# Kernel optimization log

Measured on AMD Instinct MI355X. Metric: run time of the kernel, lower is better.

Reference implementation:

```python
import jax, jax.numpy as jnp
import numpy as np

NUM_EXPERTS = 8
TOP_K = 2


def setup_inputs() -> dict:
    key = jax.random.key(0)
    ks = jax.random.split(key, 8)
    B, S, D, H, E = 4, 2048, 1024, 2048, NUM_EXPERTS
    sd = 1.0 / np.sqrt(D)
    sh = 1.0 / np.sqrt(H)
    return {
        "x": jax.random.normal(ks[0], (B, S, D), dtype=jnp.float32),
        "noise": jax.random.normal(ks[1], (B, S, E), dtype=jnp.float32),
        "router_w": jax.random.normal(ks[2], (E, D), dtype=jnp.float32) * sd,
        "router_b": jnp.zeros((E,), dtype=jnp.float32),
        "noise_w": jax.random.normal(ks[3], (E, D), dtype=jnp.float32) * sd,
        "noise_b": jnp.zeros((E,), dtype=jnp.float32),
        "w1": jax.random.normal(ks[4], (E, H, D), dtype=jnp.float32) * sd,
        "w2": jax.random.normal(ks[5], (E, D, H), dtype=jnp.float32) * sh,
        "w3": jax.random.normal(ks[6], (E, H, D), dtype=jnp.float32) * sd,
    }


def reference(x, noise, router_w, router_b, noise_w, noise_b, w1, w2, w3):
    B, S, D = x.shape
    T = B * S
    xf = x.reshape(T, D)                                  # [T, D]
    noise_f = noise.reshape(T, -1)                        # [T, E]

    # Noisy top-k router
    logits = xf @ router_w.T + router_b                   # [T, E]
    noise_logits = xf @ noise_w.T + noise_b               # [T, E]
    noisy = logits + noise_f * jax.nn.softplus(noise_logits)
    top_vals, top_idx = jax.lax.top_k(noisy, TOP_K)       # [T, K]
    sparse = jnp.full_like(noisy, -jnp.inf)
    sparse = sparse.at[jnp.arange(T)[:, None], top_idx].set(top_vals)
    gates = jax.nn.softmax(sparse, axis=-1)               # [T, E]; zero off top-k

    # Expert SwiGLU combine. Gates are exactly 0 for non-selected experts, so
    # the masked gather/scatter loop of the original equals this weighted sum.
    out = jnp.zeros_like(xf)
    for i in range(NUM_EXPERTS):
        h = jax.nn.silu(xf @ w1[i].T) * (xf @ w3[i].T)    # [T, H]
        out = out + gates[:, i:i + 1] * (h @ w2[i].T)     # [T, D]
    return out.reshape(B, S, D)
```

## Files before the change

kernel.cpp:

```cpp
#include <hip/hip_runtime.h>

typedef unsigned short u16;
typedef __attribute__((ext_vector_type(8))) __bf16 bf16x8;
typedef __attribute__((ext_vector_type(8))) short short8;
typedef __attribute__((ext_vector_type(4))) float f32x4;

#define NE 8

__device__ __forceinline__ u16 f2bf(float f) {
    union { float f; unsigned u; } v; v.f = f;
    unsigned u = v.u;
    return (u16)((u + 0x7fffu + ((u >> 16) & 1u)) >> 16);
}

__device__ __forceinline__ f32x4 mfma16(short8 a, short8 b, f32x4 c) {
    return __builtin_amdgcn_mfma_f32_16x16x32_bf16(
        __builtin_bit_cast(bf16x8, a), __builtin_bit_cast(bf16x8, b), c, 0, 0, 0);
}

__device__ __forceinline__ void gl2lds(const u16* g, u16* l) {
    __builtin_amdgcn_global_load_lds((const __attribute__((address_space(1))) void*)g,
                                     (__attribute__((address_space(3))) void*)l,
                                     16, 0, 0);
}

__global__ void cvt_kernel(const float* __restrict__ in, u16* __restrict__ out, size_t n4) {
    size_t i = (size_t)blockIdx.x * blockDim.x + threadIdx.x;
    size_t stride = (size_t)gridDim.x * blockDim.x;
    for (; i < n4; i += stride) {
        float4 v = ((const float4*)in)[i];
        ushort4 o;
        o.x = f2bf(v.x); o.y = f2bf(v.y); o.z = f2bf(v.z); o.w = f2bf(v.w);
        ((ushort4*)out)[i] = o;
    }
}

__global__ void cvt_w13_kernel(const float* __restrict__ w1, const float* __restrict__ w3,
                               u16* __restrict__ wc, int H, int D) {
    size_t n = (size_t)NE * H * (D / 4);
    size_t i = (size_t)blockIdx.x * blockDim.x + threadIdx.x;
    size_t stride = (size_t)gridDim.x * blockDim.x;
    int d4n = D / 4;
    for (; i < n; i += stride) {
        int d4 = (int)(i % d4n);
        size_t rem = i / d4n;
        int j = (int)(rem % H);
        int e = (int)(rem / H);
        float4 v1 = ((const float4*)w1)[i];
        float4 v3 = ((const float4*)w3)[i];
        ushort4 o1, o3;
        o1.x = f2bf(v1.x); o1.y = f2bf(v1.y); o1.z = f2bf(v1.z); o1.w = f2bf(v1.w);
        o3.x = f2bf(v3.x); o3.y = f2bf(v3.y); o3.z = f2bf(v3.z); o3.w = f2bf(v3.w);
        int wcrow = ((j >> 4) << 5) + (j & 15);
        size_t o = (((size_t)e * 2 * H + wcrow) * d4n + d4);
        ((ushort4*)wc)[o] = o1;
        ((ushort4*)wc)[o + (size_t)16 * d4n] = o3;
    }
}

__global__ void router_kernel(const float* __restrict__ x, const float* __restrict__ noise,
                              const float* __restrict__ rw, const float* __restrict__ rb,
                              const float* __restrict__ nw, const float* __restrict__ nb,
                              int* __restrict__ tops, float* __restrict__ gpair,
                              u16* __restrict__ xb, int T, int D) {
    int wv = threadIdx.x >> 6;
    int lane = threadIdx.x & 63;
    int t = blockIdx.x * 4 + wv;
    if (t >= T) return;

    const float4* x4 = (const float4*)(x + (size_t)t * D) + lane * 4;
    float4 xv0 = x4[0], xv1 = x4[1], xv2 = x4[2], xv3 = x4[3];

    {
        ushort4 s0, s1, s2, s3;
        s0.x = f2bf(xv0.x); s0.y = f2bf(xv0.y); s0.z = f2bf(xv0.z); s0.w = f2bf(xv0.w);
        s1.x = f2bf(xv1.x); s1.y = f2bf(xv1.y); s1.z = f2bf(xv1.z); s1.w = f2bf(xv1.w);
        s2.x = f2bf(xv2.x); s2.y = f2bf(xv2.y); s2.z = f2bf(xv2.z); s2.w = f2bf(xv2.w);
        s3.x = f2bf(xv3.x); s3.y = f2bf(xv3.y); s3.z = f2bf(xv3.z); s3.w = f2bf(xv3.w);
        ushort4* o = (ushort4*)(xb + (size_t)t * D + lane * 16);
        o[0] = s0; o[1] = s1; o[2] = s2; o[3] = s3;
    }

    float acc[2 * NE];
#pragma unroll
    for (int e = 0; e < NE; e++) {
        const float4* w4 = (const float4*)(rw + (size_t)e * D) + lane * 4;
        float4 a = w4[0], b = w4[1], c = w4[2], d = w4[3];
        acc[e] = xv0.x*a.x + xv0.y*a.y + xv0.z*a.z + xv0.w*a.w
               + xv1.x*b.x + xv1.y*b.y + xv1.z*b.z + xv1.w*b.w
               + xv2.x*c.x + xv2.y*c.y + xv2.z*c.z + xv2.w*c.w
               + xv3.x*d.x + xv3.y*d.y + xv3.z*d.z + xv3.w*d.w;
        const float4* v4 = (const float4*)(nw + (size_t)e * D) + lane * 4;
        a = v4[0]; b = v4[1]; c = v4[2]; d = v4[3];
        acc[NE + e] = xv0.x*a.x + xv0.y*a.y + xv0.z*a.z + xv0.w*a.w
                    + xv1.x*b.x + xv1.y*b.y + xv1.z*b.z + xv1.w*b.w
                    + xv2.x*c.x + xv2.y*c.y + xv2.z*c.z + xv2.w*c.w
                    + xv3.x*d.x + xv3.y*d.y + xv3.z*d.z + xv3.w*d.w;
    }
#pragma unroll
    for (int m = 1; m < 64; m <<= 1) {
#pragma unroll
        for (int k = 0; k < 2 * NE; k++) acc[k] += __shfl_xor(acc[k], m);
    }

    if (lane == 0) {
        float v0 = -1e30f, v1 = -1e30f;
        int i0 = 0, i1 = 0;
#pragma unroll
        for (int e = 0; e < NE; e++) {
            float z = acc[NE + e] + nb[e];
            float sp = (z > 20.f) ? z : log1pf(expf(z));
            float nv = acc[e] + rb[e] + noise[(size_t)t * NE + e] * sp;
            if (nv > v0) { v1 = v0; i1 = i0; v0 = nv; i0 = e; }
            else if (nv > v1) { v1 = nv; i1 = e; }
        }
        float e1 = expf(v1 - v0);
        float inv = 1.f / (1.f + e1);
        tops[t] = i0 | (i1 << 8);
        gpair[2 * t]     = inv;
        gpair[2 * t + 1] = e1 * inv;
    }
}

__global__ void build_kernel(const int* __restrict__ tops, const float* __restrict__ gpair,
                             int* __restrict__ counts, int* __restrict__ list,
                             float* __restrict__ glist, int* __restrict__ tokslot, int T) {
    int e = blockIdx.x;
    int tid = threadIdx.x, lane = tid & 63, wv = tid >> 6;
    __shared__ int wsum[4];
    __shared__ int sbase;
    if (tid == 0) sbase = 0;
    __syncthreads();
    for (int t0 = 0; t0 < T; t0 += 256) {
        int t = t0 + tid;
        int pk = tops[t];
        int i0 = pk & 0xff, i1 = (pk >> 8) & 0xff;
        bool f0 = (i0 == e), f1 = (i1 == e);
        bool f = f0 || f1;
        unsigned long long m = __ballot(f);
        int lpos = __popcll(m & (((unsigned long long)1 << lane) - 1ull));
        if (lane == 0) wsum[wv] = __popcll(m);
        __syncthreads();
        int woff = sbase;
        for (int w = 0; w < wv; w++) woff += wsum[w];
        int tot = wsum[0] + wsum[1] + wsum[2] + wsum[3];
        if (f) {
            int pos = woff + lpos;
            list[e * T + pos]  = t;
            glist[e * T + pos] = f0 ? gpair[2 * t] : gpair[2 * t + 1];
            tokslot[2 * t + (f0 ? 0 : 1)] = (e << 16) | pos;
        }
        __syncthreads();
        if (tid == 0) sbase += tot;
    }
    __syncthreads();
    if (tid == 0) counts[e] = sbase;
}

__global__ void scan_kernel(const int* __restrict__ counts, int* __restrict__ offsets,
                            int* __restrict__ bmap, int* __restrict__ nb) {
    if (threadIdx.x == 0 && blockIdx.x == 0) {
        int s = 0, t = 0;
        for (int e = 0; e < NE; e++) {
            offsets[e] = s;
            int c = counts[e];
            s += c;
            int m = (c + 127) >> 7;
            for (int i = 0; i < m; i++) bmap[t++] = (e << 16) | i;
        }
        offsets[NE] = s;
        nb[0] = t;
    }
}

__launch_bounds__(256)
__global__ void gemm1_kernel(const u16* __restrict__ xb, const u16* __restrict__ wc,
                             const int* __restrict__ counts, const int* __restrict__ offsets,
                             const int* __restrict__ list, const float* __restrict__ glist,
                             const int* __restrict__ bmap, const int* __restrict__ nb,
                             u16* __restrict__ hb, int T, int D, int H) {
    if ((int)blockIdx.y >= nb[0]) return;
    int info = bmap[blockIdx.y];
    int e = info >> 16, mblk = info & 0xffff, nblk = blockIdx.x;
    int count = counts[e];

    __shared__ u16 sA[2 * 4096];
    __shared__ u16 sB[2 * 4096];
    __shared__ int stok[128];
    __shared__ float sgate[128];

    int tid = threadIdx.x;
    int lane = tid & 63, wvi = tid >> 6;

    if (tid < 128) {
        int rr = min(mblk * 128 + tid, count - 1);
        stok[tid]  = list[e * T + rr];
        sgate[tid] = glist[e * T + rr];
    }
    __syncthreads();

    int n0 = nblk * 128;
    const u16* wcp = wc + ((size_t)e * 2 * H + n0) * D;

    int rowc = tid >> 2, col8 = (tid & 3) * 8;
    const u16* pa0 = xb + (size_t)stok[rowc] * D + col8;
    const u16* pa1 = xb + (size_t)stok[64 + rowc] * D + col8;
    const u16* pb0 = wcp + (size_t)rowc * D + col8;
    const u16* pb1 = wcp + (size_t)(64 + rowc) * D + col8;
    int lo0 = wvi * 512, lo1 = 2048 + wvi * 512;

    f32x4 acc[4][4];
#pragma unroll
    for (int mi = 0; mi < 4; mi++)
#pragma unroll
        for (int ni = 0; ni < 4; ni++) acc[mi][ni] = (f32x4)0.f;

    int wm = (wvi & 1) * 64, wn = (wvi >> 1) * 64;
    int r = lane & 15, q = lane >> 4;

#define G1_ISSUE(buf) do { \
        gl2lds(pa0, sA + (buf) * 4096 + lo0); gl2lds(pa1, sA + (buf) * 4096 + lo1); \
        gl2lds(pb0, sB + (buf) * 4096 + lo0); gl2lds(pb1, sB + (buf) * 4096 + lo1); \
        pa0 += 32; pa1 += 32; pb0 += 32; pb1 += 32; } while (0)

#define G1_COMPUTE(buf) do { \
        short8 a[4], b[4]; \
        _Pragma("unroll") \
        for (int mi = 0; mi < 4; mi++) \
            a[mi] = *(const short8*)(&sA[(buf) * 4096 + (wm + mi * 16 + r) * 32 + q * 8]); \
        _Pragma("unroll") \
        for (int ni = 0; ni < 4; ni++) \
            b[ni] = *(const short8*)(&sB[(buf) * 4096 + (wn + ni * 16 + r) * 32 + q * 8]); \
        _Pragma("unroll") \
        for (int mi = 0; mi < 4; mi++) \
            _Pragma("unroll") \
            for (int ni = 0; ni < 4; ni++) \
                acc[mi][ni] = mfma16(a[mi], b[ni], acc[mi][ni]); } while (0)

    G1_ISSUE(0);
    for (int k0 = 0; k0 < D; k0 += 64) {
        __syncthreads();
        if (k0 + 32 < D) G1_ISSUE(1);
        G1_COMPUTE(0);
        __syncthreads();
        if (k0 + 64 < D) G1_ISSUE(0);
        G1_COMPUTE(1);
    }

    int hrow0 = offsets[e];
#pragma unroll
    for (int mi = 0; mi < 4; mi++) {
#pragma unroll
        for (int g = 0; g < 2; g++) {
            int col = nblk * 64 + (wn >> 1) + g * 16 + r;
#pragma unroll
            for (int tt = 0; tt < 4; tt++) {
                int lrow = wm + mi * 16 + q * 4 + tt;
                int grow = mblk * 128 + lrow;
                if (grow < count) {
                    float v = acc[mi][2 * g][tt];
                    float hv = v / (1.f + expf(-v)) * acc[mi][2 * g + 1][tt] * sgate[lrow];
                    hb[(size_t)(hrow0 + grow) * H + col] = f2bf(hv);
                }
            }
        }
    }
}

__launch_bounds__(256)
__global__ void gemm2_kernel(const u16* __restrict__ hb, const u16* __restrict__ w2b,
                             const int* __restrict__ counts, const int* __restrict__ offsets,
                             const int* __restrict__ bmap, const int* __restrict__ nb,
                             float* __restrict__ o2, int T, int D, int H) {
    if ((int)blockIdx.y >= nb[0]) return;
    int info = bmap[blockIdx.y];
    int e = info >> 16, mblk = info & 0xffff, nblk = blockIdx.x;
    int count = counts[e];

    __shared__ u16 sA[2 * 4096];
    __shared__ u16 sB[2 * 4096];

    int tid = threadIdx.x;
    int lane = tid & 63, wvi = tid >> 6;
    int off0 = offsets[e];
    int n0 = nblk * 128;
    const u16* w2p = w2b + ((size_t)e * D + n0) * H;

    int rowc = tid >> 2, col8 = (tid & 3) * 8;
    int ra0 = min(mblk * 128 + rowc, count - 1);
    int ra1 = min(mblk * 128 + 64 + rowc, count - 1);
    const u16* pa0 = hb + (size_t)(off0 + ra0) * H + col8;
    const u16* pa1 = hb + (size_t)(off0 + ra1) * H + col8;
    const u16* pb0 = w2p + (size_t)rowc * H + col8;
    const u16* pb1 = w2p + (size_t)(64 + rowc) * H + col8;
    int lo0 = wvi * 512, lo1 = 2048 + wvi * 512;

    f32x4 acc[4][4];
#pragma unroll
    for (int mi = 0; mi < 4; mi++)
#pragma unroll
        for (int ni = 0; ni < 4; ni++) acc[mi][ni] = (f32x4)0.f;

    int wm = (wvi & 1) * 64, wn = (wvi >> 1) * 64;
    int r = lane & 15, q = lane >> 4;

#define G2_ISSUE(buf) do { \
        gl2lds(pa0, sA + (buf) * 4096 + lo0); gl2lds(pa1, sA + (buf) * 4096 + lo1); \
        gl2lds(pb0, sB + (buf) * 4096 + lo0); gl2lds(pb1, sB + (buf) * 4096 + lo1); \
        pa0 += 32; pa1 += 32; pb0 += 32; pb1 += 32; } while (0)

#define G2_COMPUTE(buf) do { \
        short8 a[4], b[4]; \
        _Pragma("unroll") \
        for (int mi = 0; mi < 4; mi++) \
            a[mi] = *(const short8*)(&sA[(buf) * 4096 + (wm + mi * 16 + r) * 32 + q * 8]); \
        _Pragma("unroll") \
        for (int ni = 0; ni < 4; ni++) \
            b[ni] = *(const short8*)(&sB[(buf) * 4096 + (wn + ni * 16 + r) * 32 + q * 8]); \
        _Pragma("unroll") \
        for (int mi = 0; mi < 4; mi++) \
            _Pragma("unroll") \
            for (int ni = 0; ni < 4; ni++) \
                acc[mi][ni] = mfma16(a[mi], b[ni], acc[mi][ni]); } while (0)

    G2_ISSUE(0);
    for (int k0 = 0; k0 < H; k0 += 64) {
        __syncthreads();
        if (k0 + 32 < H) G2_ISSUE(1);
        G2_COMPUTE(0);
        __syncthreads();
        if (k0 + 64 < H) G2_ISSUE(0);
        G2_COMPUTE(1);
    }

#pragma unroll
    for (int mi = 0; mi < 4; mi++) {
#pragma unroll
        for (int tt = 0; tt < 4; tt++) {
            int grow = mblk * 128 + wm + mi * 16 + q * 4 + tt;
            if (grow < count) {
#pragma unroll
                for (int ni = 0; ni < 4; ni++) {
                    int col = n0 + wn + ni * 16 + r;
                    o2[(size_t)(off0 + grow) * D + col] = acc[mi][ni][tt];
                }
            }
        }
    }
}

__global__ void combine_kernel(const float* __restrict__ o2, const int* __restrict__ tokslot,
                               const int* __restrict__ offsets, float* __restrict__ out, int D) {
    int t = blockIdx.x;
    int s0 = tokslot[2 * t], s1 = tokslot[2 * t + 1];
    size_t r0 = offsets[s0 >> 16] + (s0 & 0xffff);
    size_t r1 = offsets[s1 >> 16] + (s1 & 0xffff);
    int c = threadIdx.x * 4;
    float4 a = *(const float4*)(o2 + r0 * D + c);
    float4 b = *(const float4*)(o2 + r1 * D + c);
    float4 o; o.x = a.x + b.x; o.y = a.y + b.y; o.z = a.z + b.z; o.w = a.w + b.w;
    *(float4*)(out + (size_t)t * D + c) = o;
}

extern "C" void kernel_launch(void* const* d_in, const int* in_sizes, int n_in,
                              void* d_out, int out_size, void* d_ws, size_t ws_size,
                              hipStream_t stream) {
    const float* x     = (const float*)d_in[0];
    const float* noise = (const float*)d_in[1];
    const float* rw    = (const float*)d_in[2];
    const float* rb    = (const float*)d_in[3];
    const float* nw    = (const float*)d_in[4];
    const float* nb_   = (const float*)d_in[5];
    const float* w1    = (const float*)d_in[6];
    const float* w2    = (const float*)d_in[7];
    const float* w3    = (const float*)d_in[8];
    float* out = (float*)d_out;

    const int E = NE;
    const int D = in_sizes[2] / E;
    const int T = in_sizes[0] / D;
    const int H = in_sizes[6] / (E * D);

    auto al = [](size_t v) { return (v + 255) & ~(size_t)255; };
    char* p = (char*)d_ws;
    size_t o_counts  = 0;
    size_t o_offsets = 64;
    size_t o_nb      = 128;
    size_t o_bmap    = 256;
    size_t o_tslot   = al(o_bmap  + 2048);
    size_t o_list    = al(o_tslot + (size_t)2 * T * 4);
    size_t o_glist   = al(o_list  + (size_t)E * T * 4);
    size_t o_xb      = al(o_glist + (size_t)E * T * 4);
    size_t o_wc      = al(o_xb    + (size_t)T * D * 2);
    size_t o_w2b     = al(o_wc    + (size_t)E * 2 * H * D * 2);
    size_t o_hb      = al(o_w2b   + (size_t)E * D * H * 2);

    int*   counts  = (int*)(p + o_counts);
    int*   offsets = (int*)(p + o_offsets);
    int*   nblk    = (int*)(p + o_nb);
    int*   bmap    = (int*)(p + o_bmap);
    int*   tokslot = (int*)(p + o_tslot);
    int*   list    = (int*)(p + o_list);
    float* glist   = (float*)(p + o_glist);
    u16*   xb      = (u16*)(p + o_xb);
    u16*   wc      = (u16*)(p + o_wc);
    float* o2      = (float*)(p + o_wc);
    u16*   w2b     = (u16*)(p + o_w2b);
    u16*   hb      = (u16*)(p + o_hb);
    int*   tops    = (int*)(p + o_hb);
    float* gpair   = (float*)(p + o_hb + (size_t)T * 4);

    cvt_w13_kernel<<<2048, 256, 0, stream>>>(w1, w3, wc, H, D);
    cvt_kernel<<<2048, 256, 0, stream>>>(w2, w2b, (size_t)E * D * H / 4);

    router_kernel<<<(T + 3) / 4, 256, 0, stream>>>(x, noise, rw, rb, nw, nb_,
                                                   tops, gpair, xb, T, D);
    build_kernel<<<NE, 256, 0, stream>>>(tops, gpair, counts, list, glist, tokslot, T);
    scan_kernel<<<1, 64, 0, stream>>>(counts, offsets, bmap, nblk);

    int maxb = 2 * T / 128 + NE;
    dim3 g1(2 * H / 128, maxb, 1);
    gemm1_kernel<<<g1, 256, 0, stream>>>(xb, wc, counts, offsets, list, glist,
                                         bmap, nblk, hb, T, D, H);
    dim3 g2(D / 128, maxb, 1);
    gemm2_kernel<<<g2, 256, 0, stream>>>(hb, w2b, counts, offsets,
                                         bmap, nblk, o2, T, D, H);
    combine_kernel<<<T, 256, 0, stream>>>(o2, tokslot, offsets, out, D);
}
```

Measured before the change: 656.5 us.

## Enlarge grouped GEMM tiles to 256x256 with 3-stage LDS pipeline and swizzle

Both expert GEMMs move from 128x128 tiles with 256 threads to 256x256 tiles with 512 threads (8 waves), a triple-buffered global-to-LDS pipeline driven by explicit vmcnt waits and s_barrier, an XOR swizzle on LDS columns to reduce bank conflicts, and s_setprio around the MFMA bursts. The scan kernel now builds the block map in 256-row chunks. The goal is more data reuse per tile and better overlap of loads with MFMA work. In exchange there are fewer blocks, more padding waste on partial expert tiles, and higher register pressure from 128 accumulator floats per thread under a 2-blocks-per-CU launch bound.

```diff
diff --git a/kernel.cpp b/kernel.cpp
--- a/kernel.cpp
+++ b/kernel.cpp
@@ -6,6 +6,12 @@
 typedef __attribute__((ext_vector_type(4))) float f32x4;
 
 #define NE 8
+
+#define SBAR()      asm volatile("s_barrier" ::: "memory")
+#define WAIT_LGKM0() do { asm volatile("s_waitcnt lgkmcnt(0)" ::: "memory"); \
+                          __builtin_amdgcn_sched_barrier(0); } while (0)
+#define WAIT_VM4()  asm volatile("s_waitcnt vmcnt(4)" ::: "memory")
+#define WAIT_VM0()  asm volatile("s_waitcnt vmcnt(0)" ::: "memory")
 
 __device__ __forceinline__ u16 f2bf(float f) {
     union { float f; unsigned u; } v; v.f = f;
@@ -165,7 +171,7 @@
             offsets[e] = s;
             int c = counts[e];
             s += c;
-            int m = (c + 127) >> 7;
+            int m = (c + 255) >> 8;
             for (int i = 0; i < m; i++) bmap[t++] = (e << 16) | i;
         }
         offsets[NE] = s;
@@ -173,7 +179,27 @@
     }
 }
 
-__launch_bounds__(256)
+
+#define FRAG_READS(abase, bbase, af, bf, mibase) do { \
+        _Pragma("unroll") \
+        for (int mi = 0; mi < 4; mi++) \
+            af[mi] = *(const short8*)((abase) + aoff + ((mibase) + mi) * 512); \
+        if (bf##_load) { \
+            _Pragma("unroll") \
+            for (int ni = 0; ni < 4; ni++) \
+                bf[ni] = *(const short8*)((bbase) + boff + ni * 512); \
+        } } while (0)
+
+#define MFMA16X(af, bf, mibase) do { \
+        __builtin_amdgcn_s_setprio(1); \
+        _Pragma("unroll") \
+        for (int mi = 0; mi < 4; mi++) \
+            _Pragma("unroll") \
+            for (int ni = 0; ni < 4; ni++) \
+                acc[(mibase) + mi][ni] = mfma16(af[mi], bf[ni], acc[(mibase) + mi][ni]); \
+        __builtin_amdgcn_s_setprio(0); } while (0)
+
+__launch_bounds__(512, 2)
 __global__ void gemm1_kernel(const u16* __restrict__ xb, const u16* __restrict__ wc,
                              const int* __restrict__ counts, const int* __restrict__ offsets,
                              const int* __restrict__ list, const float* __restrict__ glist,
@@ -184,82 +210,99 @@
     int e = info >> 16, mblk = info & 0xffff, nblk = blockIdx.x;
     int count = counts[e];
 
-    __shared__ u16 sA[2 * 4096];
-    __shared__ u16 sB[2 * 4096];
-    __shared__ int stok[128];
-    __shared__ float sgate[128];
+    __shared__ u16 sA[3 * 8192];
+    __shared__ u16 sB[3 * 8192];
+    __shared__ int stok[256];
+    __shared__ float sgate[256];
 
     int tid = threadIdx.x;
-    int lane = tid & 63, wvi = tid >> 6;
-
-    if (tid < 128) {
-        int rr = min(mblk * 128 + tid, count - 1);
+    int lane = tid & 63, wid = tid >> 6;
+
+    if (tid < 256) {
+        int rr = min(mblk * 256 + tid, count - 1);
         stok[tid]  = list[e * T + rr];
         sgate[tid] = glist[e * T + rr];
     }
     __syncthreads();
 
-    int n0 = nblk * 128;
-    const u16* wcp = wc + ((size_t)e * 2 * H + n0) * D;
-
-    int rowc = tid >> 2, col8 = (tid & 3) * 8;
-    const u16* pa0 = xb + (size_t)stok[rowc] * D + col8;
-    const u16* pa1 = xb + (size_t)stok[64 + rowc] * D + col8;
-    const u16* pb0 = wcp + (size_t)rowc * D + col8;
-    const u16* pb1 = wcp + (size_t)(64 + rowc) * D + col8;
-    int lo0 = wvi * 512, lo1 = 2048 + wvi * 512;
-
-    f32x4 acc[4][4];
-#pragma unroll
-    for (int mi = 0; mi < 4; mi++)
+    const u16* wcp = wc + ((size_t)e * 2 * H + nblk * 256) * D;
+
+    int srow = tid >> 2, qs = tid & 3;
+    int cchk = qs ^ ((srow >> 1) & 3);
+    const u16* pa0 = xb + (size_t)stok[srow] * D + cchk * 8;
+    const u16* pa1 = xb + (size_t)stok[128 + srow] * D + cchk * 8;
+    const u16* pb0 = wcp + (size_t)srow * D + cchk * 8;
+    const u16* pb1 = wcp + (size_t)(128 + srow) * D + cchk * 8;
+    u16* dstA = sA + wid * 512;
+    u16* dstB = sB + wid * 512;
+
+    int r = lane & 15, q = lane >> 4;
+    int cq = q ^ ((r >> 1) & 3);
+    int wr = wid >> 2, wc4 = wid & 3;
+    int aoff = (wr * 128 + r) * 32 + cq * 8;
+    int boff = (wc4 * 64 + r) * 32 + cq * 8;
+
+    f32x4 acc[8][4];
+#pragma unroll
+    for (int mi = 0; mi < 8; mi++)
 #pragma unroll
         for (int ni = 0; ni < 4; ni++) acc[mi][ni] = (f32x4)0.f;
 
-    int wm = (wvi & 1) * 64, wn = (wvi >> 1) * 64;
-    int r = lane & 15, q = lane >> 4;
-
-#define G1_ISSUE(buf) do { \
-        gl2lds(pa0, sA + (buf) * 4096 + lo0); gl2lds(pa1, sA + (buf) * 4096 + lo1); \
-        gl2lds(pb0, sB + (buf) * 4096 + lo0); gl2lds(pb1, sB + (buf) * 4096 + lo1); \
-        pa0 += 32; pa1 += 32; pb0 += 32; pb1 += 32; } while (0)
-
-#define G1_COMPUTE(buf) do { \
-        short8 a[4], b[4]; \
-        _Pragma("unroll") \
-        for (int mi = 0; mi < 4; mi++) \
-            a[mi] = *(const short8*)(&sA[(buf) * 4096 + (wm + mi * 16 + r) * 32 + q * 8]); \
-        _Pragma("unroll") \
-        for (int ni = 0; ni < 4; ni++) \
-            b[ni] = *(const short8*)(&sB[(buf) * 4096 + (wn + ni * 16 + r) * 32 + q * 8]); \
-        _Pragma("unroll") \
-        for (int mi = 0; mi < 4; mi++) \
-            _Pragma("unroll") \
-            for (int ni = 0; ni < 4; ni++) \
-                acc[mi][ni] = mfma16(a[mi], b[ni], acc[mi][ni]); } while (0)
-
-    G1_ISSUE(0);
-    for (int k0 = 0; k0 < D; k0 += 64) {
-        __syncthreads();
-        if (k0 + 32 < D) G1_ISSUE(1);
-        G1_COMPUTE(0);
-        __syncthreads();
-        if (k0 + 64 < D) G1_ISSUE(0);
-        G1_COMPUTE(1);
+    gl2lds(pa0, dstA);          gl2lds(pb0, dstB);
+    gl2lds(pa1, dstA + 4096);   gl2lds(pb1, dstB + 4096);
+    pa0 += 32; pa1 += 32; pb0 += 32; pb1 += 32;
+    gl2lds(pa0, dstA + 8192);          gl2lds(pb0, dstB + 8192);
+    gl2lds(pa1, dstA + 8192 + 4096);   gl2lds(pb1, dstB + 8192 + 4096);
+    pa0 += 32; pa1 += 32; pb0 += 32; pb1 += 32;
+    WAIT_VM4();
+    SBAR();
+
+    const int nt = D >> 5;
+    int cur = 0;
+    for (int t = 0; t < nt; ++t) {
+        const u16* abase = sA + cur * 8192;
+        const u16* bbase = sB + cur * 8192;
+        int stg = cur + 2; if (stg >= 3) stg -= 3;
+        u16* asg = sA + stg * 8192 + wid * 512;
+        u16* bsg = sB + stg * 8192 + wid * 512;
+        bool st = (t + 2 < nt);
+
+        short8 af[4], bf[4];
+        const bool bf_load = true;
+        FRAG_READS(abase, bbase, af, bf, 0);
+        if (st) { gl2lds(pa0, asg); gl2lds(pb0, bsg); }
+        SBAR();
+        WAIT_LGKM0();
+        MFMA16X(af, bf, 0);
+        SBAR();
+#pragma unroll
+        for (int mi = 0; mi < 4; mi++)
+            af[mi] = *(const short8*)(abase + aoff + (4 + mi) * 512);
+        if (st) {
+            gl2lds(pa1, asg + 4096); gl2lds(pb1, bsg + 4096);
+            pa0 += 32; pa1 += 32; pb0 += 32; pb1 += 32;
+        }
+        SBAR();
+        WAIT_LGKM0();
+        MFMA16X(af, bf, 4);
+        if (st) { WAIT_VM4(); } else { WAIT_VM0(); }
+        SBAR();
+        cur++; if (cur >= 3) cur = 0;
     }
 
     int hrow0 = offsets[e];
 #pragma unroll
-    for (int mi = 0; mi < 4; mi++) {
-#pragma unroll
-        for (int g = 0; g < 2; g++) {
-            int col = nblk * 64 + (wn >> 1) + g * 16 + r;
+    for (int mi = 0; mi < 8; mi++) {
+#pragma unroll
+        for (int p = 0; p < 2; p++) {
+            int col = nblk * 128 + wc4 * 32 + p * 16 + r;
 #pragma unroll
             for (int tt = 0; tt < 4; tt++) {
-                int lrow = wm + mi * 16 + q * 4 + tt;
-                int grow = mblk * 128 + lrow;
+                int lrow = wr * 128 + mi * 16 + q * 4 + tt;
+                int grow = mblk * 256 + lrow;
                 if (grow < count) {
-                    float v = acc[mi][2 * g][tt];
-                    float hv = v / (1.f + expf(-v)) * acc[mi][2 * g + 1][tt] * sgate[lrow];
+                    float v = acc[mi][2 * p][tt];
+                    float hv = v / (1.f + expf(-v)) * acc[mi][2 * p + 1][tt] * sgate[lrow];
                     hb[(size_t)(hrow0 + grow) * H + col] = f2bf(hv);
                 }
             }
@@ -267,7 +310,7 @@
     }
 }
 
-__launch_bounds__(256)
+__launch_bounds__(512, 2)
 __global__ void gemm2_kernel(const u16* __restrict__ hb, const u16* __restrict__ w2b,
                              const int* __restrict__ counts, const int* __restrict__ offsets,
                              const int* __restrict__ bmap, const int* __restrict__ nb,
@@ -277,71 +320,88 @@
     int e = info >> 16, mblk = info & 0xffff, nblk = blockIdx.x;
     int count = counts[e];
 
-    __shared__ u16 sA[2 * 4096];
-    __shared__ u16 sB[2 * 4096];
+    __shared__ u16 sA[3 * 8192];
+    __shared__ u16 sB[3 * 8192];
 
     int tid = threadIdx.x;
-    int lane = tid & 63, wvi = tid >> 6;
+    int lane = tid & 63, wid = tid >> 6;
     int off0 = offsets[e];
-    int n0 = nblk * 128;
-    const u16* w2p = w2b + ((size_t)e * D + n0) * H;
-
-    int rowc = tid >> 2, col8 = (tid & 3) * 8;
-    int ra0 = min(mblk * 128 + rowc, count - 1);
-    int ra1 = min(mblk * 128 + 64 + rowc, count - 1);
-    const u16* pa0 = hb + (size_t)(off0 + ra0) * H + col8;
-    const u16* pa1 = hb + (size_t)(off0 + ra1) * H + col8;
-    const u16* pb0 = w2p + (size_t)rowc * H + col8;
-    const u16* pb1 = w2p + (size_t)(64 + rowc) * H + col8;
-    int lo0 = wvi * 512, lo1 = 2048 + wvi * 512;
-
-    f32x4 acc[4][4];
-#pragma unroll
-    for (int mi = 0; mi < 4; mi++)
+    const u16* w2p = w2b + ((size_t)e * D + nblk * 256) * H;
+
+    int srow = tid >> 2, qs = tid & 3;
+    int cchk = qs ^ ((srow >> 1) & 3);
+    int ra0 = min(mblk * 256 + srow, count - 1);
+    int ra1 = min(mblk * 256 + 128 + srow, count - 1);
+    const u16* pa0 = hb + (size_t)(off0 + ra0) * H + cchk * 8;
+    const u16* pa1 = hb + (size_t)(off0 + ra1) * H + cchk * 8;
+    const u16* pb0 = w2p + (size_t)srow * H + cchk * 8;
+    const u16* pb1 = w2p + (size_t)(128 + srow) * H + cchk * 8;
+    u16* dstA = sA + wid * 512;
+    u16* dstB = sB + wid * 512;
+
+    int r = lane & 15, q = lane >> 4;
+    int cq = q ^ ((r >> 1) & 3);
+    int wr = wid >> 2, wc4 = wid & 3;
+    int aoff = (wr * 128 + r) * 32 + cq * 8;
+    int boff = (wc4 * 64 + r) * 32 + cq * 8;
+
+    f32x4 acc[8][4];
+#pragma unroll
+    for (int mi = 0; mi < 8; mi++)
 #pragma unroll
         for (int ni = 0; ni < 4; ni++) acc[mi][ni] = (f32x4)0.f;
 
-    int wm = (wvi & 1) * 64, wn = (wvi >> 1) * 64;
-    int r = lane & 15, q = lane >> 4;
-
-#define G2_ISSUE(buf) do { \
-        gl2lds(pa0, sA + (buf) * 4096 + lo0); gl2lds(pa1, sA + (buf) * 4096 + lo1); \
-        gl2lds(pb0, sB + (buf) * 4096 + lo0); gl2lds(pb1, sB + (buf) * 4096 + lo1); \
-        pa0 += 32; pa1 += 32; pb0 += 32; pb1 += 32; } while (0)
-
-#define G2_COMPUTE(buf) do { \
-        short8 a[4], b[4]; \
-        _Pragma("unroll") \
-        for (int mi = 0; mi < 4; mi++) \
-            a[mi] = *(const short8*)(&sA[(buf) * 4096 + (wm + mi * 16 + r) * 32 + q * 8]); \
-        _Pragma("unroll") \
-        for (int ni = 0; ni < 4; ni++) \
-            b[ni] = *(const short8*)(&sB[(buf) * 4096 + (wn + ni * 16 + r) * 32 + q * 8]); \
-        _Pragma("unroll") \
-        for (int mi = 0; mi < 4; mi++) \
-            _Pragma("unroll") \
-            for (int ni = 0; ni < 4; ni++) \
-                acc[mi][ni] = mfma16(a[mi], b[ni], acc[mi][ni]); } while (0)
-
-    G2_ISSUE(0);
-    for (int k0 = 0; k0 < H; k0 += 64) {
-        __syncthreads();
-        if (k0 + 32 < H) G2_ISSUE(1);
-        G2_COMPUTE(0);
-        __syncthreads();
-        if (k0 + 64 < H) G2_ISSUE(0);
-        G2_COMPUTE(1);
-    }
-
-#pragma unroll
-    for (int mi = 0; mi < 4; mi++) {
+    gl2lds(pa0, dstA);          gl2lds(pb0, dstB);
+    gl2lds(pa1, dstA + 4096);   gl2lds(pb1, dstB + 4096);
+    pa0 += 32; pa1 += 32; pb0 += 32; pb1 += 32;
+    gl2lds(pa0, dstA + 8192);          gl2lds(pb0, dstB + 8192);
+    gl2lds(pa1, dstA + 8192 + 4096);   gl2lds(pb1, dstB + 8192 + 4096);
+    pa0 += 32; pa1 += 32; pb0 += 32; pb1 += 32;
+    WAIT_VM4();
+    SBAR();
+
+    const int nt = H >> 5;
+    int cur = 0;
+    for (int t = 0; t < nt; ++t) {
+        const u16* abase = sA + cur * 8192;
+        const u16* bbase = sB + cur * 8192;
+        int stg = cur + 2; if (stg >= 3) stg -= 3;
+        u16* asg = sA + stg * 8192 + wid * 512;
+        u16* bsg = sB + stg * 8192 + wid * 512;
+        bool st = (t + 2 < nt);
+
+        short8 af[4], bf[4];
+        const bool bf_load = true;
+        FRAG_READS(abase, bbase, af, bf, 0);
+        if (st) { gl2lds(pa0, asg); gl2lds(pb0, bsg); }
+        SBAR();
+        WAIT_LGKM0();
+        MFMA16X(af, bf, 0);
+        SBAR();
+#pragma unroll
+        for (int mi = 0; mi < 4; mi++)
+            af[mi] = *(const short8*)(abase + aoff + (4 + mi) * 512);
+        if (st) {
+            gl2lds(pa1, asg + 4096); gl2lds(pb1, bsg + 4096);
+            pa0 += 32; pa1 += 32; pb0 += 32; pb1 += 32;
+        }
+        SBAR();
+        WAIT_LGKM0();
+        MFMA16X(af, bf, 4);
+        if (st) { WAIT_VM4(); } else { WAIT_VM0(); }
+        SBAR();
+        cur++; if (cur >= 3) cur = 0;
+    }
+
+#pragma unroll
+    for (int mi = 0; mi < 8; mi++) {
 #pragma unroll
         for (int tt = 0; tt < 4; tt++) {
-            int grow = mblk * 128 + wm + mi * 16 + q * 4 + tt;
+            int grow = mblk * 256 + wr * 128 + mi * 16 + q * 4 + tt;
             if (grow < count) {
 #pragma unroll
                 for (int ni = 0; ni < 4; ni++) {
-                    int col = n0 + wn + ni * 16 + r;
+                    int col = nblk * 256 + wc4 * 64 + ni * 16 + r;
                     o2[(size_t)(off0 + grow) * D + col] = acc[mi][ni][tt];
                 }
             }
@@ -418,12 +478,12 @@
     build_kernel<<<NE, 256, 0, stream>>>(tops, gpair, counts, list, glist, tokslot, T);
     scan_kernel<<<1, 64, 0, stream>>>(counts, offsets, bmap, nblk);
 
-    int maxb = 2 * T / 128 + NE;
-    dim3 g1(2 * H / 128, maxb, 1);
-    gemm1_kernel<<<g1, 256, 0, stream>>>(xb, wc, counts, offsets, list, glist,
+    int maxb = 2 * T / 256 + NE;
+    dim3 g1(2 * H / 256, maxb, 1);
+    gemm1_kernel<<<g1, 512, 0, stream>>>(xb, wc, counts, offsets, list, glist,
                                          bmap, nblk, hb, T, D, H);
-    dim3 g2(D / 128, maxb, 1);
-    gemm2_kernel<<<g2, 256, 0, stream>>>(hb, w2b, counts, offsets,
+    dim3 g2(D / 256, maxb, 1);
+    gemm2_kernel<<<g2, 512, 0, stream>>>(hb, w2b, counts, offsets,
                                          bmap, nblk, o2, T, D, H);
     combine_kernel<<<T, 256, 0, stream>>>(o2, tokslot, offsets, out, D);
 }
```

Result: no change. 659.5 us (+0.5%).
